# Kernel optimization log

Hardware: AMD Instinct MI355X
Metric: run time of the kernel (lower is better)

## Reference

```python
import jax, jax.numpy as jnp
import numpy as np


def setup_inputs() -> dict:
    key = jax.random.key(0)
    k = jax.random.split(key, 5)
    B, D, T = 8, 512, 8192
    Dh = D // 8
    return {
        "x": jax.random.normal(k[0], (B, D, T), dtype=jnp.float32),
        "w1": jax.random.normal(k[1], (Dh, D), dtype=jnp.float32) * (1.0 / np.sqrt(D)),
        "b1": jax.random.normal(k[2], (Dh,), dtype=jnp.float32) * 0.01,
        "w2": jax.random.normal(k[3], (D, Dh), dtype=jnp.float32) * (1.0 / np.sqrt(Dh)),
        "b2": jax.random.normal(k[4], (D,), dtype=jnp.float32) * 0.01,
        "chunksize": 16,
    }


def reference(x, w1, b1, w2, b2, chunksize):
    # x: [B, D, T]
    B, D, T = x.shape
    pad = (T + chunksize - 1) // chunksize * chunksize - T  # static under jit
    Tp = T + pad
    xp = jnp.pad(x, ((0, 0), (0, 0), (0, pad)))
    # causal cumulative average over time
    denom = jnp.arange(1, Tp + 1, dtype=x.dtype)
    avg = jnp.cumsum(xp, axis=2) / denom  # [B, D, Tp]
    pooled = avg[:, :, chunksize - 1::chunksize]  # [B, D, Tc]
    # SE bottleneck (1x1 convs)
    h = jax.nn.relu(jnp.einsum('od,bdt->bot', w1, pooled) + b1[:, None])
    g = jax.nn.sigmoid(jnp.einsum('od,bdt->bot', w2, h) + b2[:, None])  # [B, D, Tc]
    # upsample gate to per-frame resolution and apply to residual
    up = jnp.repeat(g, chunksize, axis=2)[:, :, :T]
    return up * x
```

## Files before the change

### kernel.cpp

```cpp
#include <hip/hip_runtime.h>
#include <math.h>

#define BB 8
#define DD 512
#define DH 64
#define TT 8192
#define CS 16
#define CC 512

__device__ __forceinline__ float sigf(float v) {
    return 1.0f / (1.0f + __expf(-v));
}

__global__ __launch_bounds__(256) void k_transpose(
        const float* __restrict__ w1, const float* __restrict__ w2,
        float* __restrict__ w1t, float* __restrict__ w2t) {
    int i = blockIdx.x * 256 + threadIdx.x;
    int o = i & 63, d = i >> 6;
    w1t[i] = w1[o * DD + d];
    int o2 = i & 511, oo = i >> 9;
    w2t[i] = w2[o2 * DH + oo];
}

__global__ __launch_bounds__(256) void k_pool(
        const float* __restrict__ x, float* __restrict__ pooled) {
    const int row = blockIdx.x;
    const int t = threadIdx.x;
    const float4* xr = (const float4*)(x + (size_t)row * TT);

    __shared__ float psum[2048];
    __shared__ float wtot[4];

    #pragma unroll
    for (int k = 0; k < 8; k++) {
        float4 v = xr[t + k * 256];
        psum[t + k * 256] = (v.x + v.y) + (v.z + v.w);
    }
    __syncthreads();

    const float4* ps4 = (const float4*)psum;
    float4 q0 = ps4[2 * t];
    float4 q1 = ps4[2 * t + 1];
    float c0 = (q0.x + q0.y) + (q0.z + q0.w);
    float c1 = (q1.x + q1.y) + (q1.z + q1.w);

    float ps = c0 + c1;
    float v = ps;
    int lane = t & 63;
    #pragma unroll
    for (int off = 1; off < 64; off <<= 1) {
        float n = __shfl_up(v, off, 64);
        if (lane >= off) v += n;
    }
    int wid = t >> 6;
    if (lane == 63) wtot[wid] = v;
    __syncthreads();
    float wpre = 0.0f;
    for (int w = 0; w < wid; w++) wpre += wtot[w];
    float incl = v + wpre;
    float excl = incl - ps;
    float s0 = excl + c0;
    float s1 = s0 + c1;
    int c = 2 * t;
    float2 outv;
    outv.x = s0 / (float)(CS * (c + 1));
    outv.y = s1 / (float)(CS * (c + 2));
    ((float2*)(pooled + (size_t)row * CC))[t] = outv;
}

#define PSTR 516

__global__ __launch_bounds__(256) void k_segemm(
        const float* __restrict__ pooled,
        const float* __restrict__ w1t, const float* __restrict__ b1,
        const float* __restrict__ w2t, const float* __restrict__ b2,
        float* __restrict__ g) {
    const int b = blockIdx.y;
    const int c0 = blockIdx.x * 4;
    const int t = threadIdx.x;

    __shared__ float p[4 * PSTR];
    __shared__ float hs[DH * 4];

    {
        const float4* src = (const float4*)(pooled + (size_t)b * DD * CC + c0);
        float4 v0 = src[(size_t)t * (CC / 4)];
        float4 v1 = src[((size_t)t + 256) * (CC / 4)];
        p[0 * PSTR + t] = v0.x; p[1 * PSTR + t] = v0.y;
        p[2 * PSTR + t] = v0.z; p[3 * PSTR + t] = v0.w;
        p[0 * PSTR + t + 256] = v1.x; p[1 * PSTR + t + 256] = v1.y;
        p[2 * PSTR + t + 256] = v1.z; p[3 * PSTR + t + 256] = v1.w;
    }
    __syncthreads();

    const int o = t >> 2, c = t & 3;
    const float4* pc = (const float4*)(p + c * PSTR);
    float a0 = 0.f, a1 = 0.f, a2 = 0.f, a3 = 0.f;
    #pragma unroll 4
    for (int d4 = 0; d4 < 128; d4++) {
        float4 pv = pc[d4];
        int d = d4 * 4;
        a0 = fmaf(w1t[(d + 0) * DH + o], pv.x, a0);
        a1 = fmaf(w1t[(d + 1) * DH + o], pv.y, a1);
        a2 = fmaf(w1t[(d + 2) * DH + o], pv.z, a2);
        a3 = fmaf(w1t[(d + 3) * DH + o], pv.w, a3);
    }
    float hv = ((a0 + a1) + (a2 + a3)) + b1[o];
    hs[t] = fmaxf(hv, 0.0f);
    __syncthreads();

    float g00 = 0, g01 = 0, g02 = 0, g03 = 0;
    float g10 = 0, g11 = 0, g12 = 0, g13 = 0;
    const float4* h4 = (const float4*)hs;
    #pragma unroll 8
    for (int oo = 0; oo < DH; oo++) {
        float wv0 = w2t[oo * DD + t];
        float wv1 = w2t[oo * DD + t + 256];
        float4 h = h4[oo];
        g00 = fmaf(wv0, h.x, g00); g01 = fmaf(wv0, h.y, g01);
        g02 = fmaf(wv0, h.z, g02); g03 = fmaf(wv0, h.w, g03);
        g10 = fmaf(wv1, h.x, g10); g11 = fmaf(wv1, h.y, g11);
        g12 = fmaf(wv1, h.z, g12); g13 = fmaf(wv1, h.w, g13);
    }
    float bb0 = b2[t], bb1 = b2[t + 256];
    float4 r0, r1;
    r0.x = sigf(g00 + bb0); r0.y = sigf(g01 + bb0);
    r0.z = sigf(g02 + bb0); r0.w = sigf(g03 + bb0);
    r1.x = sigf(g10 + bb1); r1.y = sigf(g11 + bb1);
    r1.z = sigf(g12 + bb1); r1.w = sigf(g13 + bb1);
    float4* gp = (float4*)(g + (size_t)b * DD * CC + c0);
    gp[(size_t)t * (CC / 4)] = r0;
    gp[((size_t)t + 256) * (CC / 4)] = r1;
}

__global__ __launch_bounds__(256) void k_gate(
        const float* __restrict__ x, const float* __restrict__ g,
        float* __restrict__ out) {
    size_t i = (size_t)blockIdx.x * 256 + threadIdx.x;
    float4 xv = ((const float4*)x)[i];
    size_t t4  = i & (TT / 4 - 1);
    size_t row = i >> 11;
    int c = (int)(t4 >> 2);
    float gv = g[row * CC + c];
    float4 r;
    r.x = xv.x * gv; r.y = xv.y * gv; r.z = xv.z * gv; r.w = xv.w * gv;
    ((float4*)out)[i] = r;
}

extern "C" void kernel_launch(void* const* d_in, const int* in_sizes, int n_in,
                              void* d_out, int out_size, void* d_ws, size_t ws_size,
                              hipStream_t stream) {
    const float* x  = (const float*)d_in[0];
    const float* w1 = (const float*)d_in[1];
    const float* b1 = (const float*)d_in[2];
    const float* w2 = (const float*)d_in[3];
    const float* b2 = (const float*)d_in[4];
    float* out = (float*)d_out;

    char* ws = (char*)d_ws;
    float* pooled = (float*)(ws);
    float* g      = (float*)(ws + (size_t)BB * DD * CC * 4);
    float* w1t    = (float*)(ws + (size_t)2 * BB * DD * CC * 4);
    float* w2t    = (float*)(ws + (size_t)2 * BB * DD * CC * 4 + DH * DD * 4);

    k_transpose<<<dim3(32768 / 256), dim3(256), 0, stream>>>(w1, w2, w1t, w2t);
    k_pool<<<dim3(BB * DD), dim3(256), 0, stream>>>(x, pooled);
    k_segemm<<<dim3(CC / 4, BB), dim3(256), 0, stream>>>(pooled, w1t, b1, w2t, b2, g);
    k_gate<<<dim3((size_t)BB * DD * TT / 4 / 256), dim3(256), 0, stream>>>(x, g, out);
}
```

Before: 291.6 us.

## Fuse SE bottleneck GEMMs with gate application and drop weight transpose

Merges the SE GEMM kernel and the gating kernel so each block computes its gate tile into shared memory and immediately multiplies the matching x tile. It removes the global gate buffer and its round trip, and eliminates the weight-transpose kernel by reading w1 and w2 rows directly as float4. This cuts two launches, at the cost of fewer blocks streaming x, each behind a GEMM prologue, and less coalesced weight loads.

New measurement: 289.0 us. No clear change (-0.9%).

```diff
diff --git a/kernel.cpp b/kernel.cpp
--- a/kernel.cpp
+++ b/kernel.cpp
@@ -10,16 +10,6 @@
 
 __device__ __forceinline__ float sigf(float v) {
     return 1.0f / (1.0f + __expf(-v));
-}
-
-__global__ __launch_bounds__(256) void k_transpose(
-        const float* __restrict__ w1, const float* __restrict__ w2,
-        float* __restrict__ w1t, float* __restrict__ w2t) {
-    int i = blockIdx.x * 256 + threadIdx.x;
-    int o = i & 63, d = i >> 6;
-    w1t[i] = w1[o * DD + d];
-    int o2 = i & 511, oo = i >> 9;
-    w2t[i] = w2[o2 * DH + oo];
 }
 
 __global__ __launch_bounds__(256) void k_pool(
@@ -70,17 +60,19 @@
 
 #define PSTR 516
 
-__global__ __launch_bounds__(256) void k_segemm(
+__global__ __launch_bounds__(256) void k_fused(
+        const float* __restrict__ x,
         const float* __restrict__ pooled,
-        const float* __restrict__ w1t, const float* __restrict__ b1,
-        const float* __restrict__ w2t, const float* __restrict__ b2,
-        float* __restrict__ g) {
+        const float* __restrict__ w1, const float* __restrict__ b1,
+        const float* __restrict__ w2, const float* __restrict__ b2,
+        float* __restrict__ out) {
     const int b = blockIdx.y;
     const int c0 = blockIdx.x * 4;
     const int t = threadIdx.x;
 
     __shared__ float p[4 * PSTR];
     __shared__ float hs[DH * 4];
+    __shared__ float gs[DD * 4];
 
     {
         const float4* src = (const float4*)(pooled + (size_t)b * DD * CC + c0);
@@ -94,57 +86,83 @@
     __syncthreads();
 
     const int o = t >> 2, c = t & 3;
+    const float4* w1r = (const float4*)(w1 + (size_t)o * DD);
     const float4* pc = (const float4*)(p + c * PSTR);
     float a0 = 0.f, a1 = 0.f, a2 = 0.f, a3 = 0.f;
     #pragma unroll 4
     for (int d4 = 0; d4 < 128; d4++) {
+        float4 wv = w1r[d4];
         float4 pv = pc[d4];
-        int d = d4 * 4;
-        a0 = fmaf(w1t[(d + 0) * DH + o], pv.x, a0);
-        a1 = fmaf(w1t[(d + 1) * DH + o], pv.y, a1);
-        a2 = fmaf(w1t[(d + 2) * DH + o], pv.z, a2);
-        a3 = fmaf(w1t[(d + 3) * DH + o], pv.w, a3);
+        a0 = fmaf(wv.x, pv.x, a0);
+        a1 = fmaf(wv.y, pv.y, a1);
+        a2 = fmaf(wv.z, pv.z, a2);
+        a3 = fmaf(wv.w, pv.w, a3);
     }
     float hv = ((a0 + a1) + (a2 + a3)) + b1[o];
     hs[t] = fmaxf(hv, 0.0f);
     __syncthreads();
 
-    float g00 = 0, g01 = 0, g02 = 0, g03 = 0;
-    float g10 = 0, g11 = 0, g12 = 0, g13 = 0;
-    const float4* h4 = (const float4*)hs;
-    #pragma unroll 8
-    for (int oo = 0; oo < DH; oo++) {
-        float wv0 = w2t[oo * DD + t];
-        float wv1 = w2t[oo * DD + t + 256];
-        float4 h = h4[oo];
-        g00 = fmaf(wv0, h.x, g00); g01 = fmaf(wv0, h.y, g01);
-        g02 = fmaf(wv0, h.z, g02); g03 = fmaf(wv0, h.w, g03);
-        g10 = fmaf(wv1, h.x, g10); g11 = fmaf(wv1, h.y, g11);
-        g12 = fmaf(wv1, h.z, g12); g13 = fmaf(wv1, h.w, g13);
+    {
+        const float4* h4 = (const float4*)hs;
+        const float4* w2a = (const float4*)(w2 + (size_t)t * DH);
+        const float4* w2b = (const float4*)(w2 + ((size_t)t + 256) * DH);
+        float gA0 = 0, gA1 = 0, gA2 = 0, gA3 = 0;
+        float gB0 = 0, gB1 = 0, gB2 = 0, gB3 = 0;
+        #pragma unroll 4
+        for (int q = 0; q < 16; q++) {
+            float4 wa = w2a[q];
+            float4 wb = w2b[q];
+            float4 hA = h4[4 * q + 0];
+            float4 hB = h4[4 * q + 1];
+            float4 hC = h4[4 * q + 2];
+            float4 hD = h4[4 * q + 3];
+            gA0 = fmaf(wa.x, hA.x, gA0); gA0 = fmaf(wa.y, hB.x, gA0);
+            gA0 = fmaf(wa.z, hC.x, gA0); gA0 = fmaf(wa.w, hD.x, gA0);
+            gA1 = fmaf(wa.x, hA.y, gA1); gA1 = fmaf(wa.y, hB.y, gA1);
+            gA1 = fmaf(wa.z, hC.y, gA1); gA1 = fmaf(wa.w, hD.y, gA1);
+            gA2 = fmaf(wa.x, hA.z, gA2); gA2 = fmaf(wa.y, hB.z, gA2);
+            gA2 = fmaf(wa.z, hC.z, gA2); gA2 = fmaf(wa.w, hD.z, gA2);
+            gA3 = fmaf(wa.x, hA.w, gA3); gA3 = fmaf(wa.y, hB.w, gA3);
+            gA3 = fmaf(wa.z, hC.w, gA3); gA3 = fmaf(wa.w, hD.w, gA3);
+            gB0 = fmaf(wb.x, hA.x, gB0); gB0 = fmaf(wb.y, hB.x, gB0);
+            gB0 = fmaf(wb.z, hC.x, gB0); gB0 = fmaf(wb.w, hD.x, gB0);
+            gB1 = fmaf(wb.x, hA.y, gB1); gB1 = fmaf(wb.y, hB.y, gB1);
+            gB1 = fmaf(wb.z, hC.y, gB1); gB1 = fmaf(wb.w, hD.y, gB1);
+            gB2 = fmaf(wb.x, hA.z, gB2); gB2 = fmaf(wb.y, hB.z, gB2);
+            gB2 = fmaf(wb.z, hC.z, gB2); gB2 = fmaf(wb.w, hD.z, gB2);
+            gB3 = fmaf(wb.x, hA.w, gB3); gB3 = fmaf(wb.y, hB.w, gB3);
+            gB3 = fmaf(wb.z, hC.w, gB3); gB3 = fmaf(wb.w, hD.w, gB3);
+        }
+        float bbA = b2[t], bbB = b2[t + 256];
+        float4 rA, rB;
+        rA.x = sigf(gA0 + bbA); rA.y = sigf(gA1 + bbA);
+        rA.z = sigf(gA2 + bbA); rA.w = sigf(gA3 + bbA);
+        rB.x = sigf(gB0 + bbB); rB.y = sigf(gB1 + bbB);
+        rB.z = sigf(gB2 + bbB); rB.w = sigf(gB3 + bbB);
+        float4* gs4 = (float4*)gs;
+        gs4[t] = rA;
+        gs4[t + 256] = rB;
     }
-    float bb0 = b2[t], bb1 = b2[t + 256];
-    float4 r0, r1;
-    r0.x = sigf(g00 + bb0); r0.y = sigf(g01 + bb0);
-    r0.z = sigf(g02 + bb0); r0.w = sigf(g03 + bb0);
-    r1.x = sigf(g10 + bb1); r1.y = sigf(g11 + bb1);
-    r1.z = sigf(g12 + bb1); r1.w = sigf(g13 + bb1);
-    float4* gp = (float4*)(g + (size_t)b * DD * CC + c0);
-    gp[(size_t)t * (CC / 4)] = r0;
-    gp[((size_t)t + 256) * (CC / 4)] = r1;
-}
+    __syncthreads();
 
-__global__ __launch_bounds__(256) void k_gate(
-        const float* __restrict__ x, const float* __restrict__ g,
-        float* __restrict__ out) {
-    size_t i = (size_t)blockIdx.x * 256 + threadIdx.x;
-    float4 xv = ((const float4*)x)[i];
-    size_t t4  = i & (TT / 4 - 1);
-    size_t row = i >> 11;
-    int c = (int)(t4 >> 2);
-    float gv = g[row * CC + c];
-    float4 r;
-    r.x = xv.x * gv; r.y = xv.y * gv; r.z = xv.z * gv; r.w = xv.w * gv;
-    ((float4*)out)[i] = r;
+    {
+        const size_t base = (size_t)b * DD * (TT / 4) + (size_t)c0 * 4;
+        const float4* x4 = (const float4*)x + base;
+        float4* o4 = (float4*)out + base;
+        #pragma unroll 8
+        for (int k = 0; k < 32; k++) {
+            int idx = k * 256 + t;
+            int d = idx >> 4;
+            int t4 = idx & 15;
+            size_t a = (size_t)d * (TT / 4) + t4;
+            float4 xv = x4[a];
+            float gv = gs[d * 4 + (t4 >> 2)];
+            float4 r;
+            r.x = xv.x * gv; r.y = xv.y * gv;
+            r.z = xv.z * gv; r.w = xv.w * gv;
+            o4[a] = r;
+        }
+    }
 }
 
 extern "C" void kernel_launch(void* const* d_in, const int* in_sizes, int n_in,
@@ -157,14 +175,9 @@
     const float* b2 = (const float*)d_in[4];
     float* out = (float*)d_out;
 
-    char* ws = (char*)d_ws;
-    float* pooled = (float*)(ws);
-    float* g      = (float*)(ws + (size_t)BB * DD * CC * 4);
-    float* w1t    = (float*)(ws + (size_t)2 * BB * DD * CC * 4);
-    float* w2t    = (float*)(ws + (size_t)2 * BB * DD * CC * 4 + DH * DD * 4);
+    float* pooled = (float*)d_ws;
 
-    k_transpose<<<dim3(32768 / 256), dim3(256), 0, stream>>>(w1, w2, w1t, w2t);
     k_pool<<<dim3(BB * DD), dim3(256), 0, stream>>>(x, pooled);
-    k_segemm<<<dim3(CC / 4, BB), dim3(256), 0, stream>>>(pooled, w1t, b1, w2t, b2, g);
-    k_gate<<<dim3((size_t)BB * DD * TT / 4 / 256), dim3(256), 0, stream>>>(x, g, out);
+    k_fused<<<dim3(CC / 4, BB), dim3(256), 0, stream>>>(
+        x, pooled, w1, b1, w2, b2, out);
 }
```
